# Performance work log

Measured on AMD Instinct MI355X. Metric: run time of the kernel, lower is better.

Reference implementation:

```python
import jax, jax.numpy as jnp
import numpy as np

# --- constants from the module (KANLayer passes degree=3; BSplineActivation defaults) ---
K = 5          # num_control_points
DEG = 3        # degree
G = 3          # grid points (set_grid_points(3) in __init__)
LO, HI = -1.0, 1.0  # grid_range


def basis_table():
    """Precompute the shared [G, K] normalized Gaussian basis table (same for all edges)."""
    knots = np.linspace(LO - DEG * 0.1, HI + DEG * 0.1, K + DEG + 1)
    grid = np.linspace(LO, HI, G)
    bv = np.zeros((G, K), dtype=np.float32)
    for i in range(K):
        center = (knots[i + DEG // 2] + knots[i + DEG // 2 + 1]) / 2.0
        width = (knots[i + DEG + 1] - knots[i]) / 2.0
        bv[:, i] = np.exp(-(((grid - center) / width) ** 2))
    bv = bv / (bv.sum(axis=1, keepdims=True) + 1e-6)
    return jnp.asarray(bv)


def kan_layer(x, cp, bw, sw, imp, bv):
    """Fused KANLayer: x [B,I]; cp [I,J,K]; bw/sw/imp [I,J]; bv [G,K] -> [B,J]."""
    xc = jnp.clip(x, LO, HI)
    gi = (xc - LO) / (HI - LO) * (G - 1)                     # [B,I] in [0, G-1]
    lo = jnp.clip(jnp.floor(gi).astype(jnp.int32), 0, G - 1)
    hi = jnp.clip(jnp.ceil(gi).astype(jnp.int32), 0, G - 1)
    frac = (gi - lo.astype(gi.dtype))[..., None]             # [B,I,1]
    basis = bv[lo] * (1.0 - frac) + bv[hi] * frac            # [B,I,K] gather + lerp
    base = x * jax.nn.sigmoid(x)                             # SiLU base function, [B,I]
    # out[b,j] = sum_i imp[i,j] * (bw[i,j]*base[b,i] + sw[i,j]*basis[b,i,:]@cp[i,j,:])
    out = jnp.einsum('bi,ij->bj', base, imp * bw)
    out = out + jnp.einsum('bik,ijk->bj', basis, imp[:, :, None] * sw[:, :, None] * cp)
    return out


def setup_inputs() -> dict:
    key = jax.random.key(0)
    ks = jax.random.split(key, 9)
    B, D0, D1, D2 = 131072, 64, 128, 64
    return {
        'x': jax.random.normal(ks[0], (B, D0), dtype=jnp.float32),
        'cp0': jax.random.normal(ks[1], (D0, D1, K), dtype=jnp.float32) * 0.1,
        'bw0': jax.random.normal(ks[2], (D0, D1), dtype=jnp.float32),
        'sw0': jax.random.normal(ks[3], (D0, D1), dtype=jnp.float32),
        'imp0': jnp.ones((D0, D1), dtype=jnp.float32),
        'cp1': jax.random.normal(ks[4], (D1, D2, K), dtype=jnp.float32) * 0.1,
        'bw1': jax.random.normal(ks[5], (D1, D2), dtype=jnp.float32),
        'sw1': jax.random.normal(ks[6], (D1, D2), dtype=jnp.float32),
        'imp1': jnp.ones((D1, D2), dtype=jnp.float32),
    }


def reference(x, cp0, bw0, sw0, imp0, cp1, bw1, sw1, imp1):
    bv = basis_table()
    h = kan_layer(x, cp0, bw0, sw0, imp0, bv)
    return kan_layer(h, cp1, bw1, sw1, imp1, bv)
```

## Files before the change

### kernel.cpp

```cpp
#include <hip/hip_runtime.h>
#include <math.h>

typedef __attribute__((ext_vector_type(8))) _Float16 f16x8;
typedef __attribute__((ext_vector_type(2))) _Float16 f16x2;
typedef __attribute__((ext_vector_type(4))) float f32x4;


#define TPB 256
#define BM  128
#define HSTRIDE 272
#define W_OFF   34816
#define LDS_TOT (34816 + 16384)

__global__ __launch_bounds__(TPB, 2) void kan_mfma_kernel(
    const float* __restrict__ x, const _Float16* __restrict__ W0t,
    const _Float16* __restrict__ W1t, const float* __restrict__ bias0,
    const float* __restrict__ bias1, float* __restrict__ out)
{
    __shared__ char smem[LDS_TOT];
    const int tid  = threadIdx.x;
    const int lane = tid & 63;
    const int wid  = tid >> 6;
    const int gq   = lane >> 4;
    const int lm   = lane & 15;
    const int wavebase = wid * 32;
    const long rowbase = (long)blockIdx.x * BM;

#if __has_builtin(__builtin_amdgcn_cvt_pkrtz)
    auto pk2 = [](float a, float b) -> f16x2 {
        return (f16x2)__builtin_amdgcn_cvt_pkrtz(a, b);
    };
#else
    auto pk2 = [](float a, float b) -> f16x2 {
        return f16x2{(_Float16)a, (_Float16)b};
    };
#endif
#if __has_builtin(__builtin_amdgcn_rcpf)
    auto frcp = [](float a) -> float { return __builtin_amdgcn_rcpf(a); };
#else
    auto frcp = [](float a) -> float { return 1.0f / a; };
#endif

    auto buildFeats4 = [&](const float* v, f16x8* dst) {
        union U { f16x8 v8; f16x2 h2[4]; } u0, u1, u2, u3;
        #pragma unroll
        for (int q = 0; q < 4; ++q) {
            float va = v[2 * q], vb = v[2 * q + 1];
            float ba = va * frcp(1.0f + __expf(-va));
            float bb = vb * frcp(1.0f + __expf(-vb));
            float ga = fminf(fmaxf(va, -1.f), 1.f) + 1.f;
            float gb = fminf(fmaxf(vb, -1.f), 1.f) + 1.f;
            float s1a = (ga >= 1.f) ? 1.f : 0.f;
            float s1b = (gb >= 1.f) ? 1.f : 0.f;
            float sga = (ga >= 1.f) ? ga : 0.f;
            float sgb = (gb >= 1.f) ? gb : 0.f;
            u0.h2[q] = pk2(ba, bb);
            u1.h2[q] = pk2(ga, gb);
            u2.h2[q] = pk2(s1a, s1b);
            u3.h2[q] = pk2(sga, sgb);
        }
        dst[0] = u0.v8; dst[1] = u1.v8; dst[2] = u2.v8; dst[3] = u3.v8;
    };

    float b0v[8], b1v[4];
    #pragma unroll
    for (int nf = 0; nf < 8; ++nf) b0v[nf] = bias0[nf * 16 + lm];
    #pragma unroll
    for (int nf = 0; nf < 4; ++nf) b1v[nf] = bias1[nf * 16 + lm];

    float v0[2][8], v1[2][8];
    #pragma unroll
    for (int mi = 0; mi < 2; ++mi) {
        const float* xp = x + (rowbase + wavebase + mi * 16 + lm) * 64 + gq * 8;
        float4 a0 = *(const float4*)(xp);
        float4 a1 = *(const float4*)(xp + 4);
        float4 a2 = *(const float4*)(xp + 32);
        float4 a3 = *(const float4*)(xp + 36);
        v0[mi][0]=a0.x; v0[mi][1]=a0.y; v0[mi][2]=a0.z; v0[mi][3]=a0.w;
        v0[mi][4]=a1.x; v0[mi][5]=a1.y; v0[mi][6]=a1.z; v0[mi][7]=a1.w;
        v1[mi][0]=a2.x; v1[mi][1]=a2.y; v1[mi][2]=a2.z; v1[mi][3]=a2.w;
        v1[mi][4]=a3.x; v1[mi][5]=a3.y; v1[mi][6]=a3.z; v1[mi][7]=a3.w;
    }

    f32x4 acc[2][8] = {};
    {
        const char* w0 = (const char*)W0t;
        const int lb0 = (gq * 128 + lm) * 16;

        {
            float4 pa = *(const float4*)(w0 + tid * 32);
            float4 pb = *(const float4*)(w0 + tid * 32 + 16);
            *(float4*)(smem + W_OFF + tid * 32)      = pa;
            *(float4*)(smem + W_OFF + tid * 32 + 16) = pb;
        }
        f16x8 fr[2][4];
        buildFeats4(v0[0], fr[0]);
        buildFeats4(v0[1], fr[1]);
        __syncthreads();

        float4 wr0, wr1;
#define L0_STEP(S, C) do {                                                    \
        if ((S) < 7) {                                                        \
            wr0 = *(const float4*)(w0 + ((S) + 1) * 8192 + tid * 32);         \
            wr1 = *(const float4*)(w0 + ((S) + 1) * 8192 + tid * 32 + 16);    \
        }                                                                     \
        const char* wb = smem + W_OFF + ((S) & 1) * 8192;                     \
        f16x8 bt[8];                                                          \
        _Pragma("unroll")                                                     \
        for (int nf = 0; nf < 8; ++nf)                                        \
            bt[nf] = *(const f16x8*)(wb + lb0 + nf * 256);                    \
        _Pragma("unroll")                                                     \
        for (int mi = 0; mi < 2; ++mi) {                                      \
            f16x8 a = fr[mi][C];                                              \
            _Pragma("unroll")                                                 \
            for (int nf = 0; nf < 8; ++nf)                                    \
                acc[mi][nf] = __builtin_amdgcn_mfma_f32_16x16x32_f16(         \
                    a, bt[nf], acc[mi][nf], 0, 0, 0);                         \
        }                                                                     \
        if ((S) < 7) {                                                        \
            char* nb = smem + W_OFF + (((S) + 1) & 1) * 8192;                 \
            *(float4*)(nb + tid * 32)      = wr0;                             \
            *(float4*)(nb + tid * 32 + 16) = wr1;                             \
        }                                                                     \
        __syncthreads();                                                      \
    } while (0)

        L0_STEP(0, 0); L0_STEP(1, 1); L0_STEP(2, 2); L0_STEP(3, 3);
        buildFeats4(v1[0], fr[0]);
        buildFeats4(v1[1], fr[1]);
        L0_STEP(4, 0); L0_STEP(5, 1); L0_STEP(6, 2); L0_STEP(7, 3);
#undef L0_STEP
    }

    {
        const char* w1 = (const char*)W1t;
        float4 p0 = *(const float4*)(w1 + tid * 16);
        #pragma unroll
        for (int mi = 0; mi < 2; ++mi)
            #pragma unroll
            for (int nf = 0; nf < 8; ++nf)
                #pragma unroll
                for (int rg = 0; rg < 4; ++rg)
                    *(_Float16*)(smem + (wavebase + mi * 16 + gq * 4 + rg) * HSTRIDE
                                 + (nf * 16 + lm) * 2) = (_Float16)(acc[mi][nf][rg] + b0v[nf]);
        __syncthreads();
        *(float4*)(smem + W_OFF + tid * 16) = p0;
        __syncthreads();
    }

    f32x4 accO[2][4] = {};
    {
        const char* w1 = (const char*)W1t;
        const int lb1 = (gq * 64 + lm) * 16;
        f16x8 fr[2][4];
        float4 wr0;

#define L1_STEP(CI, C) do {                                                   \
        if ((CI) < 15)                                                        \
            wr0 = *(const float4*)(w1 + ((CI) + 1) * 4096 + tid * 16);        \
        const char* wb = smem + W_OFF + ((CI) & 1) * 8192;                    \
        f16x8 bt[4];                                                          \
        _Pragma("unroll")                                                     \
        for (int nf = 0; nf < 4; ++nf)                                        \
            bt[nf] = *(const f16x8*)(wb + lb1 + nf * 256);                    \
        _Pragma("unroll")                                                     \
        for (int mi = 0; mi < 2; ++mi) {                                      \
            f16x8 a = fr[mi][C];                                              \
            _Pragma("unroll")                                                 \
            for (int nf = 0; nf < 4; ++nf)                                    \
                accO[mi][nf] = __builtin_amdgcn_mfma_f32_16x16x32_f16(        \
                    a, bt[nf], accO[mi][nf], 0, 0, 0);                        \
        }                                                                     \
        if ((CI) < 15)                                                        \
            *(float4*)(smem + W_OFF + (((CI) + 1) & 1) * 8192 + tid * 16) = wr0; \
        __syncthreads();                                                      \
    } while (0)

#define L1_FEATS(HALF, IH) do {                                               \
        _Pragma("unroll")                                                     \
        for (int mi = 0; mi < 2; ++mi) {                                      \
            const char* hrow = smem + (wavebase + mi * 16 + lm) * HSTRIDE;    \
            f16x8 hv = *(const f16x8*)(hrow + ((HALF) * 64 + (IH) * 32 + gq * 8) * 2); \
            float v[8];                                                       \
            _Pragma("unroll")                                                 \
            for (int e = 0; e < 8; ++e) v[e] = (float)hv[e];                  \
            buildFeats4(v, fr[mi]);                                           \
        }                                                                     \
    } while (0)

        L1_FEATS(0, 0);
        L1_STEP(0, 0);  L1_STEP(1, 1);  L1_STEP(2, 2);  L1_STEP(3, 3);
        L1_FEATS(0, 1);
        L1_STEP(4, 0);  L1_STEP(5, 1);  L1_STEP(6, 2);  L1_STEP(7, 3);
        L1_FEATS(1, 0);
        L1_STEP(8, 0);  L1_STEP(9, 1);  L1_STEP(10, 2); L1_STEP(11, 3);
        L1_FEATS(1, 1);
        L1_STEP(12, 0); L1_STEP(13, 1); L1_STEP(14, 2); L1_STEP(15, 3);
#undef L1_STEP
#undef L1_FEATS
    }

    float* og = out + (rowbase + wavebase) * 64;
    #pragma unroll
    for (int mi = 0; mi < 2; ++mi)
        #pragma unroll
        for (int nf = 0; nf < 4; ++nf)
            #pragma unroll
            for (int rg = 0; rg < 4; ++rg)
                og[(mi * 16 + gq * 4 + rg) * 64 + nf * 16 + lm] = accO[mi][nf][rg] + b1v[nf];
}

__global__ __launch_bounds__(256) void kan_combine_w(
    const float* __restrict__ cp0, const float* __restrict__ bw0,
    const float* __restrict__ sw0, const float* __restrict__ imp0,
    const float* __restrict__ cp1, const float* __restrict__ bw1,
    const float* __restrict__ sw1, const float* __restrict__ imp1,
    _Float16* __restrict__ W0t, _Float16* __restrict__ W1t,
    float* __restrict__ bias0, float* __restrict__ bias1)
{
    float bvv[3][5];
    #pragma unroll
    for (int g = 0; g < 3; ++g) {
        float gv = (float)g - 1.0f;
        float e[5]; float s = 0.f;
        #pragma unroll
        for (int i = 0; i < 5; ++i) {
            float cc = -0.8125f + 0.325f * (float)i;
            float d  = (gv - cc) * (1.0f / 0.65f);
            e[i] = __expf(-d * d); s += e[i];
        }
        float inv = 1.0f / (s + 1e-6f);
        #pragma unroll
        for (int i = 0; i < 5; ++i) bvv[g][i] = e[i] * inv;
    }

    auto wval = [&](const float* cp, float bw, float sw, float imp, int q) -> float {
        if (q == 0) return imp * bw;
        float P0 = 0.f, Q0 = 0.f, P1 = 0.f, Q1 = 0.f;
        #pragma unroll
        for (int c = 0; c < 5; ++c) {
            P0 += cp[c] * bvv[0][c];
            Q0 += cp[c] * (bvv[1][c] - bvv[0][c]);
            P1 += cp[c] * (2.f * bvv[1][c] - bvv[2][c]);
            Q1 += cp[c] * (bvv[2][c] - bvv[1][c]);
        }
        float r = (q == 1) ? Q0 : (q == 2) ? (P1 - P0) : (Q1 - Q0);
        return imp * sw * r;
    };
    auto p0val = [&](const float* cp) -> float {
        float P0 = 0.f;
        #pragma unroll
        for (int c = 0; c < 5; ++c) P0 += cp[c] * bvv[0][c];
        return P0;
    };

    const int bx = blockIdx.x;
    const int t  = threadIdx.x;

    if (bx < 256) {
        int f = bx * 256 + t;
        if (f < 32768) {
            int e = f & 7, n = (f >> 3) & 127, g = (f >> 10) & 3, s = f >> 12;
            int ih = s >> 2, q = s & 3;
            int i = ih * 32 + g * 8 + e;
            int edge = i * 128 + n;
            W0t[f] = (_Float16)wval(cp0 + edge * 5, bw0[edge], sw0[edge], imp0[edge], q);
        } else {
            int f2 = f - 32768;
            int e = f2 & 7, n = (f2 >> 3) & 63, g = (f2 >> 9) & 3;
            int tq = f2 >> 11;
            int half = tq >> 3, s = tq & 7;
            int ih = s >> 2, q = s & 3;
            int i2 = half * 64 + ih * 32 + g * 8 + e;
            int edge = i2 * 64 + n;
            W1t[f2] = (_Float16)wval(cp1 + edge * 5, bw1[edge], sw1[edge], imp1[edge], q);
        }
    } else if (bx < 272) {
        __shared__ float part[256];
        int bb = bx - 256;
        int jj = t >> 5, split = t & 31;
        int j = bb * 8 + jj;
        float s = 0.f;
        #pragma unroll
        for (int k = 0; k < 2; ++k) {
            int i = split * 2 + k;
            int edge = i * 128 + j;
            s += imp0[edge] * sw0[edge] * p0val(cp0 + edge * 5);
        }
        part[t] = s;
        __syncthreads();
        if (t < 8) {
            float acc = 0.f;
            #pragma unroll
            for (int k = 0; k < 32; ++k) acc += part[t * 32 + k];
            bias0[bb * 8 + t] = acc;
        }
    } else {
        __shared__ float part[256];
        int bb = bx - 272;
        int jj = t >> 6, split = t & 63;
        int j = bb * 4 + jj;
        float s = 0.f;
        #pragma unroll
        for (int k = 0; k < 2; ++k) {
            int i2 = split * 2 + k;
            int edge = i2 * 64 + j;
            s += imp1[edge] * sw1[edge] * p0val(cp1 + edge * 5);
        }
        part[t] = s;
        __syncthreads();
        if (t < 4) {
            float acc = 0.f;
            #pragma unroll
            for (int k = 0; k < 64; ++k) acc += part[t * 64 + k];
            bias1[bb * 4 + t] = acc;
        }
    }
}

#define NTHR 256
#define JT 32
#define WS8 8

#define STAGE_L0(JBASE) do {                                                  \
    _Pragma("unroll")                                                         \
    for (int p = 0; p < 8; ++p) {                                             \
        int idx = tid + p * NTHR;                                             \
        int i  = idx >> 5;                                                    \
        int jj = idx & 31;                                                    \
        int e  = i * 128 + (JBASE) + jj;                                      \
        float im = imp0[e];                                                   \
        float wb = bw0[e] * im;                                               \
        float ws = sw0[e] * im;                                               \
        const float* cp = cp0 + e * 5;                                        \
        float* wp = wbuf + idx * WS8;                                         \
        wp[0] = wb;                                                           \
        wp[1] = ws * cp[0]; wp[2] = ws * cp[1]; wp[3] = ws * cp[2];           \
        wp[4] = ws * cp[3]; wp[5] = ws * cp[4];                               \
    }                                                                         \
} while (0)

#define STAGE_L1(IBASE, JBASE) do {                                           \
    _Pragma("unroll")                                                         \
    for (int p = 0; p < 8; ++p) {                                             \
        int idx = tid + p * NTHR;                                             \
        int ii = idx >> 5;                                                    \
        int jj = idx & 31;                                                    \
        int e  = ((IBASE) + ii) * 64 + (JBASE) + jj;                          \
        float im = imp1[e];                                                   \
        float wb = bw1[e] * im;                                               \
        float ws = sw1[e] * im;                                               \
        const float* cp = cp1 + e * 5;                                        \
        float* wp = wbuf + idx * WS8;                                         \
        wp[0] = wb;                                                           \
        wp[1] = ws * cp[0]; wp[2] = ws * cp[1]; wp[3] = ws * cp[2];           \
        wp[4] = ws * cp[3]; wp[5] = ws * cp[4];                               \
    }                                                                         \
} while (0)

#define COMPUTE_TILE(ACC) do {                                                \
    _Pragma("unroll 2")                                                       \
    for (int i = 0; i < 64; ++i) {                                            \
        float v  = vbuf[i][tid];                                              \
        float sg = 1.0f / (1.0f + __expf(-v));                                \
        float base = v * sg;                                                  \
        float xc = fminf(fmaxf(v, -1.0f), 1.0f);                              \
        float gi = xc + 1.0f;                                                 \
        int lo = (int)gi; lo = (lo > 2) ? 2 : lo;                             \
        float fr = gi - (float)lo;                                            \
        int hi = (fr > 0.0f) ? (lo + 1) : lo;                                 \
        float b0 = bvt[lo][0]; b0 += (bvt[hi][0] - b0) * fr;                  \
        float b1 = bvt[lo][1]; b1 += (bvt[hi][1] - b1) * fr;                  \
        float b2 = bvt[lo][2]; b2 += (bvt[hi][2] - b2) * fr;                  \
        float b3 = bvt[lo][3]; b3 += (bvt[hi][3] - b3) * fr;                  \
        float b4 = bvt[lo][4]; b4 += (bvt[hi][4] - b4) * fr;                  \
        const float* wr = wbuf + i * (JT * WS8);                              \
        _Pragma("unroll")                                                     \
        for (int jj = 0; jj < JT; ++jj) {                                     \
            const float* wp = wr + jj * WS8;                                  \
            float a = ACC[jj];                                                \
            a = fmaf(wp[0], base, a);                                         \
            a = fmaf(wp[1], b0, a);                                           \
            a = fmaf(wp[2], b1, a);                                           \
            a = fmaf(wp[3], b2, a);                                           \
            a = fmaf(wp[4], b3, a);                                           \
            a = fmaf(wp[5], b4, a);                                           \
            ACC[jj] = a;                                                      \
        }                                                                     \
    }                                                                         \
} while (0)

__global__ __launch_bounds__(NTHR) void kan_fused_kernel(
    const float* __restrict__ x,
    const float* __restrict__ cp0, const float* __restrict__ bw0,
    const float* __restrict__ sw0, const float* __restrict__ imp0,
    const float* __restrict__ cp1, const float* __restrict__ bw1,
    const float* __restrict__ sw1, const float* __restrict__ imp1,
    float* __restrict__ out)
{
    __shared__ float vbuf[64][NTHR + 1];
    __shared__ float wbuf[64 * JT * WS8];
    __shared__ float bvt[3][8];

    const int tid = threadIdx.x;

    if (tid < 3) {
        float gv = -1.0f + (float)tid;
        float e[5];
        float s = 0.0f;
        #pragma unroll
        for (int i = 0; i < 5; ++i) {
            float c = -0.8125f + 0.325f * (float)i;
            float d = (gv - c) * (1.0f / 0.65f);
            e[i] = expf(-d * d);
            s += e[i];
        }
        float inv = 1.0f / (s + 1e-6f);
        #pragma unroll
        for (int i = 0; i < 5; ++i) bvt[tid][i] = e[i] * inv;
    }

    {
        const float4* xg = (const float4*)(x + (size_t)blockIdx.x * (NTHR * 64));
        #pragma unroll
        for (int it = 0; it < 16; ++it) {
            int e4 = tid + it * NTHR;
            float4 v = xg[e4];
            int r  = e4 >> 4;
            int ib = (e4 & 15) << 2;
            vbuf[ib + 0][r] = v.x;
            vbuf[ib + 1][r] = v.y;
            vbuf[ib + 2][r] = v.z;
            vbuf[ib + 3][r] = v.w;
        }
    }
    __syncthreads();

    float h0[32] = {}, h1[32] = {}, h2[32] = {}, h3[32] = {};
    STAGE_L0(0);   __syncthreads(); COMPUTE_TILE(h0); __syncthreads();
    STAGE_L0(32);  __syncthreads(); COMPUTE_TILE(h1); __syncthreads();
    STAGE_L0(64);  __syncthreads(); COMPUTE_TILE(h2); __syncthreads();
    STAGE_L0(96);  __syncthreads(); COMPUTE_TILE(h3); __syncthreads();

    #pragma unroll
    for (int i = 0; i < 32; ++i) vbuf[i][tid] = h0[i];
    #pragma unroll
    for (int i = 0; i < 32; ++i) vbuf[32 + i][tid] = h1[i];

    float o0[32] = {}, o1[32] = {};
    STAGE_L1(0, 0);   __syncthreads(); COMPUTE_TILE(o0); __syncthreads();
    STAGE_L1(0, 32);  __syncthreads(); COMPUTE_TILE(o1); __syncthreads();

    #pragma unroll
    for (int i = 0; i < 32; ++i) vbuf[i][tid] = h2[i];
    #pragma unroll
    for (int i = 0; i < 32; ++i) vbuf[32 + i][tid] = h3[i];

    STAGE_L1(64, 0);  __syncthreads(); COMPUTE_TILE(o0); __syncthreads();
    STAGE_L1(64, 32); __syncthreads(); COMPUTE_TILE(o1);

    float4* og = (float4*)(out + (size_t)blockIdx.x * (NTHR * 64) + (size_t)tid * 64);
    #pragma unroll
    for (int q = 0; q < 8; ++q)
        og[q] = make_float4(o0[4 * q + 0], o0[4 * q + 1], o0[4 * q + 2], o0[4 * q + 3]);
    #pragma unroll
    for (int q = 0; q < 8; ++q)
        og[8 + q] = make_float4(o1[4 * q + 0], o1[4 * q + 1], o1[4 * q + 2], o1[4 * q + 3]);
}

extern "C" void kernel_launch(void* const* d_in, const int* in_sizes, int n_in,
                              void* d_out, int out_size, void* d_ws, size_t ws_size,
                              hipStream_t stream) {
    const float* x    = (const float*)d_in[0];
    const float* cp0  = (const float*)d_in[1];
    const float* bw0  = (const float*)d_in[2];
    const float* sw0  = (const float*)d_in[3];
    const float* imp0 = (const float*)d_in[4];
    const float* cp1  = (const float*)d_in[5];
    const float* bw1  = (const float*)d_in[6];
    const float* sw1  = (const float*)d_in[7];
    const float* imp1 = (const float*)d_in[8];
    float* out = (float*)d_out;

    const int B = in_sizes[0] / 64;
    const size_t need = 65536 * sizeof(_Float16) + 192 * sizeof(float);

    if (ws_size >= need && (B % BM) == 0) {
        _Float16* W0t = (_Float16*)d_ws;
        _Float16* W1t = W0t + 32768;
        float* bias0 = (float*)(W1t + 32768);
        float* bias1 = bias0 + 128;
        kan_combine_w<<<288, 256, 0, stream>>>(cp0, bw0, sw0, imp0,
                                               cp1, bw1, sw1, imp1,
                                               W0t, W1t, bias0, bias1);
        kan_mfma_kernel<<<B / BM, TPB, 0, stream>>>(x, W0t, W1t, bias0, bias1, out);
    } else {
        kan_fused_kernel<<<B / NTHR, NTHR, 0, stream>>>(
            x, cp0, bw0, sw0, imp0, cp1, bw1, sw1, imp1, out);
    }
}
```

Before: 37.58 us.

## Stage full weight matrices in LDS once and double block size

The block now has 512 threads and 256 rows. The whole 64KB layer-0 and layer-1 weight matrices are loaded into LDS in one bulk copy instead of being streamed in double-buffered 8KB chunks, which removes the per-step __syncthreads in both GEMM loops. The hidden-activation buffer moves to an offset after the weights. Total LDS use rises to about 135KB per block, which together with the 512-thread blocks limits occupancy, and the single bulk preload is exposed latency rather than overlapped with compute.

```diff
diff --git a/kernel.cpp b/kernel.cpp
--- a/kernel.cpp
+++ b/kernel.cpp
@@ -6,11 +6,11 @@
 typedef __attribute__((ext_vector_type(4))) float f32x4;
 
 
-#define TPB 256
-#define BM  128
+#define TPB 512
+#define BM  256
 #define HSTRIDE 272
-#define W_OFF   34816
-#define LDS_TOT (34816 + 16384)
+#define H_OFF   65536
+#define LDS_TOT (65536 + 256 * HSTRIDE)
 
 __global__ __launch_bounds__(TPB, 2) void kan_mfma_kernel(
     const float* __restrict__ x, const _Float16* __restrict__ W0t,
@@ -84,27 +84,24 @@
 
     f32x4 acc[2][8] = {};
     {
-        const char* w0 = (const char*)W0t;
+        f16x8 fr[2][4];
+        {
+            const float4* w0g = (const float4*)W0t;
+            float4 st[8];
+            #pragma unroll
+            for (int p = 0; p < 8; ++p) st[p] = w0g[tid * 8 + p];
+            buildFeats4(v0[0], fr[0]);
+            buildFeats4(v0[1], fr[1]);
+            #pragma unroll
+            for (int p = 0; p < 8; ++p)
+                *(float4*)(smem + tid * 128 + p * 16) = st[p];
+        }
+        __syncthreads();
+
         const int lb0 = (gq * 128 + lm) * 16;
 
-        {
-            float4 pa = *(const float4*)(w0 + tid * 32);
-            float4 pb = *(const float4*)(w0 + tid * 32 + 16);
-            *(float4*)(smem + W_OFF + tid * 32)      = pa;
-            *(float4*)(smem + W_OFF + tid * 32 + 16) = pb;
-        }
-        f16x8 fr[2][4];
-        buildFeats4(v0[0], fr[0]);
-        buildFeats4(v0[1], fr[1]);
-        __syncthreads();
-
-        float4 wr0, wr1;
 #define L0_STEP(S, C) do {                                                    \
-        if ((S) < 7) {                                                        \
-            wr0 = *(const float4*)(w0 + ((S) + 1) * 8192 + tid * 32);         \
-            wr1 = *(const float4*)(w0 + ((S) + 1) * 8192 + tid * 32 + 16);    \
-        }                                                                     \
-        const char* wb = smem + W_OFF + ((S) & 1) * 8192;                     \
+        const char* wb = smem + (S) * 8192;                                   \
         f16x8 bt[8];                                                          \
         _Pragma("unroll")                                                     \
         for (int nf = 0; nf < 8; ++nf)                                        \
@@ -117,12 +114,6 @@
                 acc[mi][nf] = __builtin_amdgcn_mfma_f32_16x16x32_f16(         \
                     a, bt[nf], acc[mi][nf], 0, 0, 0);                         \
         }                                                                     \
-        if ((S) < 7) {                                                        \
-            char* nb = smem + W_OFF + (((S) + 1) & 1) * 8192;                 \
-            *(float4*)(nb + tid * 32)      = wr0;                             \
-            *(float4*)(nb + tid * 32 + 16) = wr1;                             \
-        }                                                                     \
-        __syncthreads();                                                      \
     } while (0)
 
         L0_STEP(0, 0); L0_STEP(1, 1); L0_STEP(2, 2); L0_STEP(3, 3);
@@ -133,32 +124,33 @@
     }
 
     {
-        const char* w1 = (const char*)W1t;
-        float4 p0 = *(const float4*)(w1 + tid * 16);
+        const float4* w1g = (const float4*)W1t;
+        float4 st[8];
+        #pragma unroll
+        for (int p = 0; p < 8; ++p) st[p] = w1g[tid * 8 + p];
         #pragma unroll
         for (int mi = 0; mi < 2; ++mi)
             #pragma unroll
             for (int nf = 0; nf < 8; ++nf)
                 #pragma unroll
                 for (int rg = 0; rg < 4; ++rg)
-                    *(_Float16*)(smem + (wavebase + mi * 16 + gq * 4 + rg) * HSTRIDE
+                    *(_Float16*)(smem + H_OFF
+                                 + (wavebase + mi * 16 + gq * 4 + rg) * HSTRIDE
                                  + (nf * 16 + lm) * 2) = (_Float16)(acc[mi][nf][rg] + b0v[nf]);
         __syncthreads();
-        *(float4*)(smem + W_OFF + tid * 16) = p0;
+        #pragma unroll
+        for (int p = 0; p < 8; ++p)
+            *(float4*)(smem + tid * 128 + p * 16) = st[p];
         __syncthreads();
     }
 
     f32x4 accO[2][4] = {};
     {
-        const char* w1 = (const char*)W1t;
         const int lb1 = (gq * 64 + lm) * 16;
         f16x8 fr[2][4];
-        float4 wr0;
 
 #define L1_STEP(CI, C) do {                                                   \
-        if ((CI) < 15)                                                        \
-            wr0 = *(const float4*)(w1 + ((CI) + 1) * 4096 + tid * 16);        \
-        const char* wb = smem + W_OFF + ((CI) & 1) * 8192;                    \
+        const char* wb = smem + (CI) * 4096;                                  \
         f16x8 bt[4];                                                          \
         _Pragma("unroll")                                                     \
         for (int nf = 0; nf < 4; ++nf)                                        \
@@ -171,15 +163,12 @@
                 accO[mi][nf] = __builtin_amdgcn_mfma_f32_16x16x32_f16(        \
                     a, bt[nf], accO[mi][nf], 0, 0, 0);                        \
         }                                                                     \
-        if ((CI) < 15)                                                        \
-            *(float4*)(smem + W_OFF + (((CI) + 1) & 1) * 8192 + tid * 16) = wr0; \
-        __syncthreads();                                                      \
     } while (0)
 
 #define L1_FEATS(HALF, IH) do {                                               \
         _Pragma("unroll")                                                     \
         for (int mi = 0; mi < 2; ++mi) {                                      \
-            const char* hrow = smem + (wavebase + mi * 16 + lm) * HSTRIDE;    \
+            const char* hrow = smem + H_OFF + (wavebase + mi * 16 + lm) * HSTRIDE; \
             f16x8 hv = *(const f16x8*)(hrow + ((HALF) * 64 + (IH) * 32 + gq * 8) * 2); \
             float v[8];                                                       \
             _Pragma("unroll")                                                 \
```

Measured after the change: 47.73 us. 1.27x slower.
